# Kernel optimization log

Hardware: AMD Instinct MI355X
Metric: run time of the kernel (lower is better)

Reference implementation:

```python
import jax, jax.numpy as jnp
import numpy as np

D_MODEL = 512
D_STATE = 128
D_CONV = 4
EXPAND = 2
HEADDIM = 64
NGROUPS = 1
D_INNER = EXPAND * D_MODEL            # 1024
NHEADS = D_INNER // HEADDIM           # 16
CONV_DIM = D_INNER + 2 * NGROUPS * D_STATE   # 1280
D_IN_PROJ = 2 * D_INNER + 2 * NGROUPS * D_STATE + NHEADS  # 2320
EPS = 1e-5


def _silu(v):
    return v * jax.nn.sigmoid(v)


def setup_inputs() -> dict:
    key = jax.random.key(0)
    ks = jax.random.split(key, 8)
    B, L = 2, 1024
    x = jax.random.normal(ks[0], (B, L, D_MODEL), jnp.float32)
    in_proj_w = jax.random.normal(ks[1], (D_IN_PROJ, D_MODEL), jnp.float32) * (D_MODEL ** -0.5)
    conv_w = jax.random.normal(ks[2], (CONV_DIM, D_CONV), jnp.float32) * (D_CONV ** -0.5)
    conv_b = jnp.zeros((CONV_DIM,), jnp.float32)
    # dt_bias = softplus^-1(dt) for dt ~ U[1e-3, 0.1]  (Mamba2 init)
    dt = jax.random.uniform(ks[3], (NHEADS,), jnp.float32, 0.001, 0.1)
    dt_bias = jnp.log(jnp.expm1(dt))
    A_log = jnp.log(jax.random.uniform(ks[4], (NHEADS,), jnp.float32, 1.0, 16.0))
    D = jnp.ones((NHEADS,), jnp.float32)
    norm_w = jnp.ones((D_INNER,), jnp.float32)
    out_proj_w = jax.random.normal(ks[5], (D_MODEL, D_INNER), jnp.float32) * (D_INNER ** -0.5)
    return dict(x=x, in_proj_w=in_proj_w, conv_w=conv_w, conv_b=conv_b,
                dt_bias=dt_bias, A_log=A_log, D=D, norm_w=norm_w, out_proj_w=out_proj_w)


def _mamba2(x, in_proj_w, conv_w, conv_b, dt_bias, A_log, D, norm_w, out_proj_w):
    Bb, L, _ = x.shape
    # input projection -> [z | xBC | dt]
    zxbcdt = jnp.einsum('bld,ed->ble', x, in_proj_w)          # (B,L,2320)
    z = zxbcdt[..., :D_INNER]                                  # (B,L,1024)
    xBC = zxbcdt[..., D_INNER:D_INNER + CONV_DIM]              # (B,L,1280)
    dt = jax.nn.softplus(zxbcdt[..., D_INNER + CONV_DIM:] + dt_bias)  # (B,L,H)
    # causal depthwise conv1d over L + SiLU
    lhs = jnp.transpose(xBC, (0, 2, 1))                        # (B,C,L)
    rhs = conv_w[:, None, :]                                   # (C,1,K)
    conv = jax.lax.conv_general_dilated(
        lhs, rhs, window_strides=(1,), padding=[(D_CONV - 1, 0)],
        dimension_numbers=('NCH', 'OIH', 'NCH'), feature_group_count=CONV_DIM)
    xBC = _silu(jnp.transpose(conv, (0, 2, 1)) + conv_b)       # (B,L,1280)
    xs = xBC[..., :D_INNER].reshape(Bb, L, NHEADS, HEADDIM)    # (B,L,H,P)
    Bmat = xBC[..., D_INNER:D_INNER + D_STATE]                 # (B,L,N) ngroups=1
    Cmat = xBC[..., D_INNER + D_STATE:]                        # (B,L,N)
    # selective scan: h_t = exp(dt_t*A)*h_{t-1} + (dt_t*x_t) outer B_t ; y_t = C_t . h_t
    A = -jnp.exp(A_log)                                        # (H,)
    dA = jnp.exp(dt * A)                                       # (B,L,H)
    dx = dt[..., None] * xs                                    # (B,L,H,P)

    def step(h, inp):
        dA_t, dx_t, B_t, C_t = inp                             # (B,H),(B,H,P),(B,N),(B,N)
        h = h * dA_t[..., None, None] + dx_t[..., None] * B_t[:, None, None, :]
        y = jnp.einsum('bhpn,bn->bhp', h, C_t)
        return h, y

    h0 = jnp.zeros((Bb, NHEADS, HEADDIM, D_STATE), x.dtype)
    _, ys = jax.lax.scan(step, h0, (jnp.moveaxis(dA, 1, 0), jnp.moveaxis(dx, 1, 0),
                                    jnp.moveaxis(Bmat, 1, 0), jnp.moveaxis(Cmat, 1, 0)))
    y = jnp.moveaxis(ys, 0, 1) + xs * D[None, None, :, None]   # (B,L,H,P)
    y = y.reshape(Bb, L, D_INNER)
    # gated RMSNorm: rmsnorm(y * silu(z)) * w
    g = y * _silu(z)
    g = g * jax.lax.rsqrt(jnp.mean(g * g, axis=-1, keepdims=True) + EPS) * norm_w
    return jnp.einsum('ble,de->bld', g, out_proj_w)            # (B,L,d_model)


def reference(x, in_proj_w, conv_w, conv_b, dt_bias, A_log, D, norm_w, out_proj_w):
    return _mamba2(x, in_proj_w, conv_w, conv_b, dt_bias, A_log, D, norm_w, out_proj_w)
```

## Files before the change

kernel.cpp:

```cpp
#include <hip/hip_runtime.h>
#include <math.h>

#define BATCH 2
#define SEQ 1024
#define DM 512
#define DI 1024
#define DS 128
#define NH 16
#define HD 64
#define CONVD 1280
#define DPROJ 2320
#define ROWS (BATCH*SEQ)
#define NCH 16
#define CHK 64
#define NPAD 2432

typedef unsigned short u16;
typedef unsigned int   u32;
typedef u16   u16x4 __attribute__((ext_vector_type(4)));
typedef u16   u16x8 __attribute__((ext_vector_type(8)));
typedef short bf16x8 __attribute__((ext_vector_type(8)));
typedef float f32x4 __attribute__((ext_vector_type(4)));

__device__ __forceinline__ u16 f2bf(float f) {
    u32 u = __float_as_uint(f);
    return (u16)((u + 0x7fffu + ((u >> 16) & 1u)) >> 16);
}
__device__ __forceinline__ float bf2f(u16 h) {
    return __uint_as_float(((u32)h) << 16);
}
__device__ __forceinline__ void gl_lds16(const u16* g, u16* lds) {
    __builtin_amdgcn_global_load_lds((const __attribute__((address_space(1))) void*)g,
                                     (__attribute__((address_space(3))) void*)lds,
                                     16, 0, 0);
}

__device__ __forceinline__ int swz_off(int row, int q, int SLROW) {
    return (row*SLROW + (q ^ (row & 7)))*8;
}
template<int SLROW>
__device__ __forceinline__ void stage64(const u16* gbase, int gstride, u16* lds, int tid) {
    #pragma unroll
    for (int j = 0; j < (64*SLROW)/256; ++j) {
        int slot = j*256 + tid;
        int row = slot / SLROW;
        int pos = slot % SLROW;
        gl_lds16(gbase + (size_t)row*gstride + (pos ^ (row & 7))*8, lds + slot*8);
    }
}

__device__ __forceinline__ void cvt_blk(const float* __restrict__ src,
                                        u16* __restrict__ dst,
                                        int blk, int n_src, int n_total) {
    int idx = (blk*256 + threadIdx.x)*8;
    if (idx >= n_total) return;
    u16x8 o;
    if (idx + 8 <= n_src) {
        float4 a = *reinterpret_cast<const float4*>(src + idx);
        float4 b = *reinterpret_cast<const float4*>(src + idx + 4);
        o[0]=f2bf(a.x); o[1]=f2bf(a.y); o[2]=f2bf(a.z); o[3]=f2bf(a.w);
        o[4]=f2bf(b.x); o[5]=f2bf(b.y); o[6]=f2bf(b.z); o[7]=f2bf(b.w);
    } else {
        #pragma unroll
        for (int e = 0; e < 8; ++e)
            o[e] = (idx + e < n_src) ? f2bf(src[idx + e]) : (u16)0;
    }
    *reinterpret_cast<u16x8*>(dst + idx) = o;
}

__global__ __launch_bounds__(256) void k_prep(const float* __restrict__ x,
                                              const float* __restrict__ W,
                                              const float* __restrict__ Wo,
                                              const float* __restrict__ dt_bias,
                                              const float* __restrict__ A_log,
                                              u16* __restrict__ xb,
                                              u16* __restrict__ Wb,
                                              u16* __restrict__ Wob,
                                              float* __restrict__ dtb,
                                              float* __restrict__ abuf) {
    int bid = blockIdx.x;
    if (bid < 512) { cvt_blk(x, xb, bid, ROWS*DM, ROWS*DM); return; }
    if (bid < 1120) { cvt_blk(W, Wb, bid-512, DPROJ*DM, NPAD*DM); return; }
    if (bid < 1376) { cvt_blk(Wo, Wob, bid-1120, DM*DI, DM*DI); return; }
    int wave = threadIdx.x >> 6, lane = threadIdx.x & 63;
    int row = (bid-1376)*4 + wave;
    int h = lane & 15, part = lane >> 4;
    const float* xr = x + (size_t)row * DM + part*128;
    const float* wr = W + (size_t)(DI + CONVD + h) * DM + part*128;
    float acc = 0.f;
    #pragma unroll 4
    for (int j = 0; j < 32; ++j) {
        float4 xv = *reinterpret_cast<const float4*>(xr + j*4);
        float4 wv = *reinterpret_cast<const float4*>(wr + j*4);
        acc += xv.x*wv.x + xv.y*wv.y + xv.z*wv.z + xv.w*wv.w;
    }
    acc += __shfl_xor(acc, 16);
    acc += __shfl_xor(acc, 32);
    if (part == 0) {
        float v = acc + dt_bias[h];
        float dt = (v > 20.f) ? v : log1pf(expf(v));
        dtb[row*NH + h]  = dt;
        abuf[row*NH + h] = dt * (-expf(A_log[h]));
    }
}

template<int BM, int BN, int K, bool BF16OUT>
__global__ __launch_bounds__(256) void k_gemm(const u16* __restrict__ A,
                                              const u16* __restrict__ B,
                                              void* __restrict__ Cv,
                                              int ldc, int ncols) {
    constexpr int WTM = BM/2, WTN = BN/2, FM = WTM/16, FN = WTN/16;
    constexpr int CA = BM*4/256, CB = BN*4/256;
    __shared__ u16 As[BM*32];
    __shared__ u16 Bs[BN*32];
    int tid  = threadIdx.x;
    int lane = tid & 63, wave = tid >> 6;
    int wr = wave >> 1, wc = wave & 1;
    size_t bm = (size_t)blockIdx.y * BM, bn = (size_t)blockIdx.x * BN;

    const u16* srcA[CA]; u16* dstA[CA];
    #pragma unroll
    for (int j = 0; j < CA; ++j) {
        int i = j*256 + tid;
        int row = i >> 2, q = (i & 3) ^ ((row >> 1) & 3);
        srcA[j] = A + (bm + row) * (size_t)K + q*8;
        dstA[j] = As + i*8;
    }
    const u16* srcB[CB]; u16* dstB[CB];
    #pragma unroll
    for (int j = 0; j < CB; ++j) {
        int i = j*256 + tid;
        int row = i >> 2, q = (i & 3) ^ ((row >> 1) & 3);
        srcB[j] = B + (bn + row) * (size_t)K + q*8;
        dstB[j] = Bs + i*8;
    }

    int kq = lane >> 4;
    int aoff[FM], boff[FN];
    #pragma unroll
    for (int fi = 0; fi < FM; ++fi) {
        int row = wr*WTM + fi*16 + (lane & 15);
        aoff[fi] = (row*4 + (kq ^ ((row >> 1) & 3))) * 8;
    }
    #pragma unroll
    for (int fj = 0; fj < FN; ++fj) {
        int row = wc*WTN + fj*16 + (lane & 15);
        boff[fj] = (row*4 + (kq ^ ((row >> 1) & 3))) * 8;
    }

    f32x4 acc[FM][FN];
    #pragma unroll
    for (int fi = 0; fi < FM; ++fi)
        #pragma unroll
        for (int fj = 0; fj < FN; ++fj)
            acc[fi][fj] = (f32x4){0.f, 0.f, 0.f, 0.f};

    for (int k0 = 0; k0 < K; k0 += 32) {
        __syncthreads();
        #pragma unroll
        for (int j = 0; j < CA; ++j) gl_lds16(srcA[j] + k0, dstA[j]);
        #pragma unroll
        for (int j = 0; j < CB; ++j) gl_lds16(srcB[j] + k0, dstB[j]);
        __syncthreads();
        bf16x8 av[FM], bv[FN];
        #pragma unroll
        for (int fi = 0; fi < FM; ++fi)
            av[fi] = *reinterpret_cast<const bf16x8*>(As + aoff[fi]);
        #pragma unroll
        for (int fj = 0; fj < FN; ++fj)
            bv[fj] = *reinterpret_cast<const bf16x8*>(Bs + boff[fj]);
        #pragma unroll
        for (int fi = 0; fi < FM; ++fi)
            #pragma unroll
            for (int fj = 0; fj < FN; ++fj)
                acc[fi][fj] = __builtin_amdgcn_mfma_f32_16x16x32_bf16(
                    av[fi], bv[fj], acc[fi][fj], 0, 0, 0);
    }

    #pragma unroll
    for (int fi = 0; fi < FM; ++fi) {
        size_t grow0 = bm + wr*WTM + fi*16 + (lane >> 4)*4;
        #pragma unroll
        for (int fj = 0; fj < FN; ++fj) {
            size_t gcol = bn + wc*WTN + fj*16 + (lane & 15);
            if ((int)gcol < ncols) {
                #pragma unroll
                for (int r = 0; r < 4; ++r) {
                    if constexpr (BF16OUT)
                        ((u16*)Cv)[(grow0 + r)*ldc + gcol] = f2bf(acc[fi][fj][r]);
                    else
                        ((float*)Cv)[(grow0 + r)*ldc + gcol] = acc[fi][fj][r];
                }
            }
        }
    }
}

__global__ __launch_bounds__(320) void k_conv(const u16* __restrict__ zx,
                                              const float* __restrict__ cw,
                                              const float* __restrict__ cb,
                                              u16* __restrict__ convo) {
    int row = blockIdx.x;
    int l   = row & (SEQ-1);
    int c0  = threadIdx.x * 4;

    const float4* cw4 = reinterpret_cast<const float4*>(cw);
    float4 w0 = cw4[c0+0], w1 = cw4[c0+1], w2 = cw4[c0+2], w3 = cw4[c0+3];
    const float* wa0 = &w0.x; const float* wa1 = &w1.x;
    const float* wa2 = &w2.x; const float* wa3 = &w3.x;

    float4 bv = *reinterpret_cast<const float4*>(cb + c0);
    float acc0 = bv.x, acc1 = bv.y, acc2 = bv.z, acc3 = bv.w;

    #pragma unroll
    for (int k = 0; k < 4; ++k) {
        int lk = l - 3 + k;
        if (lk < 0) continue;
        u16x4 v = *reinterpret_cast<const u16x4*>(zx + (size_t)(row-3+k)*DPROJ + DI + c0);
        acc0 += bf2f(v[0]) * wa0[k];
        acc1 += bf2f(v[1]) * wa1[k];
        acc2 += bf2f(v[2]) * wa2[k];
        acc3 += bf2f(v[3]) * wa3[k];
    }
    u16x4 o;
    o[0] = f2bf(acc0 / (1.f + expf(-acc0)));
    o[1] = f2bf(acc1 / (1.f + expf(-acc1)));
    o[2] = f2bf(acc2 / (1.f + expf(-acc2)));
    o[3] = f2bf(acc3 / (1.f + expf(-acc3)));
    *reinterpret_cast<u16x4*>(convo + (size_t)row*CONVD + c0) = o;
}

__global__ __launch_bounds__(256) void k_chunk_state(
    const u16* __restrict__ convo, const float* __restrict__ dtb,
    const float* __restrict__ abuf, u16* __restrict__ Sb,
    float* __restrict__ Pbuf) {
    int blk = blockIdx.x;
    int c  = blk & (NCH-1);
    int h  = (blk >> 4) & (NH-1);
    int b  = blk >> 8;
    int row0 = b*SEQ + c*CHK;
    int tid = threadIdx.x, lane = tid & 63, wave = tid >> 6;
    int wr = wave >> 1, wc = wave & 1;

    __shared__ u16 xsT[64*64];
    __shared__ u16 BT[128*64];
    __shared__ float s_coef[CHK];

    int st = tid >> 2, q = tid & 3;
    const u16* r = convo + (size_t)(row0 + st)*CONVD;
    u16x8 xa = *reinterpret_cast<const u16x8*>(r + h*HD + q*16);
    u16x8 xc = *reinterpret_cast<const u16x8*>(r + h*HD + q*16 + 8);
    u16x8 b0 = *reinterpret_cast<const u16x8*>(r + DI + q*32);
    u16x8 b1 = *reinterpret_cast<const u16x8*>(r + DI + q*32 + 8);
    u16x8 b2 = *reinterpret_cast<const u16x8*>(r + DI + q*32 + 16);
    u16x8 b3 = *reinterpret_cast<const u16x8*>(r + DI + q*32 + 24);

    if (tid < CHK) {
        float v = abuf[(size_t)(row0 + tid)*NH + h];
        #pragma unroll
        for (int off = 1; off < 64; off <<= 1) {
            float o = __shfl_up(v, off);
            if (tid >= off) v += o;
        }
        float vend = __shfl(v, 63);
        float dt = dtb[(size_t)(row0 + tid)*NH + h];
        s_coef[tid] = dt * expf(vend - v);
        if (tid == 63) Pbuf[blk] = expf(vend);
    }
    __syncthreads();

    float cf = s_coef[st];
    #pragma unroll
    for (int e = 0; e < 16; ++e) {
        int p = q*16 + e;
        u16 xv = (e < 8) ? xa[e] : xc[e-8];
        xsT[(p*8 + ((st>>3) ^ (p&7)))*8 + (st&7)] = f2bf(cf * bf2f(xv));
    }
    #pragma unroll
    for (int e = 0; e < 32; ++e) {
        int n = q*32 + e;
        u16 bvv = (e < 8) ? b0[e] : (e < 16) ? b1[e-8] : (e < 24) ? b2[e-16] : b3[e-24];
        BT[(n*8 + ((st>>3) ^ (n&7)))*8 + (st&7)] = bvv;
    }
    __syncthreads();

    int kq = lane >> 4, fr = lane & 15;
    f32x4 acc[2][4];
    #pragma unroll
    for (int fi = 0; fi < 2; ++fi)
        #pragma unroll
        for (int fj = 0; fj < 4; ++fj)
            acc[fi][fj] = (f32x4){0.f,0.f,0.f,0.f};

    #pragma unroll
    for (int ks = 0; ks < 2; ++ks) {
        bf16x8 av[2], bv[4];
        #pragma unroll
        for (int fi = 0; fi < 2; ++fi)
            av[fi] = *reinterpret_cast<const bf16x8*>(xsT + swz_off(wr*32 + fi*16 + fr, ks*4 + kq, 8));
        #pragma unroll
        for (int fj = 0; fj < 4; ++fj)
            bv[fj] = *reinterpret_cast<const bf16x8*>(BT + swz_off(wc*64 + fj*16 + fr, ks*4 + kq, 8));
        #pragma unroll
        for (int fi = 0; fi < 2; ++fi)
            #pragma unroll
            for (int fj = 0; fj < 4; ++fj)
                acc[fi][fj] = __builtin_amdgcn_mfma_f32_16x16x32_bf16(av[fi], bv[fj], acc[fi][fj], 0,0,0);
    }

    u16* outp = Sb + (size_t)blk*(HD*DS);
    #pragma unroll
    for (int fi = 0; fi < 2; ++fi)
        #pragma unroll
        for (int rr = 0; rr < 4; ++rr) {
            int p = wr*32 + fi*16 + kq*4 + rr;
            #pragma unroll
            for (int fj = 0; fj < 4; ++fj) {
                int n = wc*64 + fj*16 + fr;
                outp[(size_t)p*DS + n] = f2bf(acc[fi][fj][rr]);
            }
        }
}

__global__ __launch_bounds__(256) void k_state_pass(u16* __restrict__ Sb,
                                                    const float* __restrict__ Pbuf) {
    int bh = blockIdx.x >> 3, seg = blockIdx.x & 7;
    int off = seg*1024 + threadIdx.x*4;
    u16x4 s[NCH];
    #pragma unroll
    for (int cc = 0; cc < NCH; ++cc)
        s[cc] = *reinterpret_cast<const u16x4*>(Sb + ((size_t)(bh*NCH + cc))*(HD*DS) + off);
    float hr[4] = {0.f,0.f,0.f,0.f};
    #pragma unroll
    for (int cc = 0; cc < NCH; ++cc) {
        u16x4 w = { f2bf(hr[0]), f2bf(hr[1]), f2bf(hr[2]), f2bf(hr[3]) };
        *reinterpret_cast<u16x4*>(Sb + ((size_t)(bh*NCH + cc))*(HD*DS) + off) = w;
        float P = Pbuf[bh*NCH + cc];
        #pragma unroll
        for (int j = 0; j < 4; ++j) hr[j] = hr[j]*P + bf2f(s[cc][j]);
    }
}

__global__ __launch_bounds__(256) void k_chunk_out(
    const u16* __restrict__ convo, const float* __restrict__ dtb,
    const float* __restrict__ abuf, const u16* __restrict__ Sb,
    const float* __restrict__ Dp, u16* __restrict__ ybuf) {
    int blk = blockIdx.x;
    int c  = blk & (NCH-1);
    int h  = (blk >> 4) & (NH-1);
    int b  = blk >> 8;
    int row0 = b*SEQ + c*CHK;
    int tid = threadIdx.x, lane = tid & 63, wave = tid >> 6;
    int wr = wave >> 1, wc = wave & 1;

    __shared__ u16 Ct[64*128];
    __shared__ u16 Bh[64*128];
    __shared__ u16 Mt[64*64];
    __shared__ u16 dxT[64*64];
    __shared__ float s_cum[CHK];
    __shared__ float s_dt[CHK];

    const u16* cbase = convo + (size_t)row0*CONVD;

    stage64<16>(cbase + DI + DS, CONVD, Ct, tid);
    stage64<16>(cbase + DI,      CONVD, Bh, tid);

    int st = tid >> 2, q = tid & 3;
    u16x8 xr0 = *reinterpret_cast<const u16x8*>(cbase + (size_t)st*CONVD + h*HD + q*16);
    u16x8 xr1 = *reinterpret_cast<const u16x8*>(cbase + (size_t)st*CONVD + h*HD + q*16 + 8);

    if (tid < CHK) {
        float v = abuf[(size_t)(row0 + tid)*NH + h];
        #pragma unroll
        for (int off = 1; off < 64; off <<= 1) {
            float o = __shfl_up(v, off);
            if (tid >= off) v += o;
        }
        s_cum[tid] = v;
        s_dt[tid] = dtb[(size_t)(row0 + tid)*NH + h];
    }
    __syncthreads();

    #pragma unroll
    for (int e = 0; e < 16; ++e) {
        int p = q*16 + e;
        u16 xv = (e < 8) ? xr0[e] : xr1[e-8];
        dxT[(p*8 + ((st>>3) ^ (p&7)))*8 + (st&7)] = xv;
    }

    int kq = lane >> 4, fr = lane & 15;

    f32x4 macc[2][2];
    #pragma unroll
    for (int fi = 0; fi < 2; ++fi)
        #pragma unroll
        for (int fj = 0; fj < 2; ++fj)
            macc[fi][fj] = (f32x4){0.f,0.f,0.f,0.f};
    #pragma unroll
    for (int ks = 0; ks < 4; ++ks) {
        bf16x8 av[2], bv[2];
        #pragma unroll
        for (int fi = 0; fi < 2; ++fi)
            av[fi] = *reinterpret_cast<const bf16x8*>(Ct + swz_off(wr*32 + fi*16 + fr, ks*4 + kq, 16));
        #pragma unroll
        for (int fj = 0; fj < 2; ++fj)
            bv[fj] = *reinterpret_cast<const bf16x8*>(Bh + swz_off(wc*32 + fj*16 + fr, ks*4 + kq, 16));
        #pragma unroll
        for (int fi = 0; fi < 2; ++fi)
            #pragma unroll
            for (int fj = 0; fj < 2; ++fj)
                macc[fi][fj] = __builtin_amdgcn_mfma_f32_16x16x32_bf16(av[fi], bv[fj], macc[fi][fj], 0,0,0);
    }

    #pragma unroll
    for (int fi = 0; fi < 2; ++fi)
        #pragma unroll
        for (int rr = 0; rr < 4; ++rr) {
            int t = wr*32 + fi*16 + kq*4 + rr;
            float cumt = s_cum[t];
            #pragma unroll
            for (int fj = 0; fj < 2; ++fj) {
                int s = wc*32 + fj*16 + fr;
                float val = (s <= t) ? macc[fi][fj][rr] * expf(cumt - s_cum[s]) * s_dt[s] : 0.f;
                Mt[(t*8 + ((s>>3) ^ (t&7)))*8 + (s&7)] = f2bf(val);
            }
        }
    __syncthreads();

    stage64<16>(Sb + (size_t)blk*(HD*DS), DS, Bh, tid);

    f32x4 accY[2][2];
    #pragma unroll
    for (int fi = 0; fi < 2; ++fi)
        #pragma unroll
        for (int fj = 0; fj < 2; ++fj)
            accY[fi][fj] = (f32x4){0.f,0.f,0.f,0.f};
    #pragma unroll
    for (int ks = 0; ks < 2; ++ks) {
        bf16x8 av[2], bv[2];
        #pragma unroll
        for (int fi = 0; fi < 2; ++fi)
            av[fi] = *reinterpret_cast<const bf16x8*>(Mt + swz_off(wr*32 + fi*16 + fr, ks*4 + kq, 8));
        #pragma unroll
        for (int fj = 0; fj < 2; ++fj)
            bv[fj] = *reinterpret_cast<const bf16x8*>(dxT + swz_off(wc*32 + fj*16 + fr, ks*4 + kq, 8));
        #pragma unroll
        for (int fi = 0; fi < 2; ++fi)
            #pragma unroll
            for (int fj = 0; fj < 2; ++fj)
                accY[fi][fj] = __builtin_amdgcn_mfma_f32_16x16x32_bf16(av[fi], bv[fj], accY[fi][fj], 0,0,0);
    }
    __syncthreads();

    f32x4 accD[2][2];
    #pragma unroll
    for (int fi = 0; fi < 2; ++fi)
        #pragma unroll
        for (int fj = 0; fj < 2; ++fj)
            accD[fi][fj] = (f32x4){0.f,0.f,0.f,0.f};
    #pragma unroll
    for (int ks = 0; ks < 4; ++ks) {
        bf16x8 av[2], bv[2];
        #pragma unroll
        for (int fi = 0; fi < 2; ++fi)
            av[fi] = *reinterpret_cast<const bf16x8*>(Ct + swz_off(wr*32 + fi*16 + fr, ks*4 + kq, 16));
        #pragma unroll
        for (int fj = 0; fj < 2; ++fj)
            bv[fj] = *reinterpret_cast<const bf16x8*>(Bh + swz_off(wc*32 + fj*16 + fr, ks*4 + kq, 16));
        #pragma unroll
        for (int fi = 0; fi < 2; ++fi)
            #pragma unroll
            for (int fj = 0; fj < 2; ++fj)
                accD[fi][fj] = __builtin_amdgcn_mfma_f32_16x16x32_bf16(av[fi], bv[fj], accD[fi][fj], 0,0,0);
    }

    float Dv = Dp[h];
    #pragma unroll
    for (int fi = 0; fi < 2; ++fi)
        #pragma unroll
        for (int rr = 0; rr < 4; ++rr) {
            int t = wr*32 + fi*16 + kq*4 + rr;
            float et = expf(s_cum[t]);
            #pragma unroll
            for (int fj = 0; fj < 2; ++fj) {
                int p = wc*32 + fj*16 + fr;
                float xs = bf2f(cbase[(size_t)t*CONVD + h*HD + p]);
                float y = accY[fi][fj][rr] + et*accD[fi][fj][rr] + Dv*xs;
                ybuf[(size_t)(row0 + t)*DI + h*HD + p] = f2bf(y);
            }
        }
}

__global__ __launch_bounds__(256) void k_gate(const u16* __restrict__ zx,
                                              const u16* __restrict__ ybuf,
                                              const float* __restrict__ nw,
                                              u16* __restrict__ g) {
    int row = blockIdx.x;
    int t = threadIdx.x;
    const u16* zr = zx + (size_t)row*DPROJ;
    const u16* yr = ybuf + (size_t)row*DI;

    u16x4 zv = *reinterpret_cast<const u16x4*>(zr + t*4);
    u16x4 yv = *reinterpret_cast<const u16x4*>(yr + t*4);
    float gv[4];
    float ss = 0.f;
    #pragma unroll
    for (int j = 0; j < 4; ++j) {
        float z = bf2f(zv[j]), y = bf2f(yv[j]);
        float sz = z / (1.f + expf(-z));
        float gg = y * sz;
        gv[j] = gg;
        ss += gg*gg;
    }
    ss += __shfl_xor(ss, 1);
    ss += __shfl_xor(ss, 2);
    ss += __shfl_xor(ss, 4);
    ss += __shfl_xor(ss, 8);
    ss += __shfl_xor(ss, 16);
    ss += __shfl_xor(ss, 32);
    __shared__ float ls[4];
    if ((t & 63) == 0) ls[t >> 6] = ss;
    __syncthreads();
    float tot = ls[0] + ls[1] + ls[2] + ls[3];
    float scale = rsqrtf(tot * (1.f/DI) + 1e-5f);

    float4 nv = *reinterpret_cast<const float4*>(nw + t*4);
    const float* na = &nv.x;
    u16x4 og = { f2bf(gv[0]*scale*na[0]), f2bf(gv[1]*scale*na[1]),
                 f2bf(gv[2]*scale*na[2]), f2bf(gv[3]*scale*na[3]) };
    *reinterpret_cast<u16x4*>(g + (size_t)row*DI + t*4) = og;
}

extern "C" void kernel_launch(void* const* d_in, const int* in_sizes, int n_in,
                              void* d_out, int out_size, void* d_ws, size_t ws_size,
                              hipStream_t stream) {
    const float* x         = (const float*)d_in[0];
    const float* in_proj_w = (const float*)d_in[1];
    const float* conv_w    = (const float*)d_in[2];
    const float* conv_b    = (const float*)d_in[3];
    const float* dt_bias   = (const float*)d_in[4];
    const float* A_log     = (const float*)d_in[5];
    const float* Dp        = (const float*)d_in[6];
    const float* norm_w    = (const float*)d_in[7];
    const float* out_proj_w= (const float*)d_in[8];
    float* out = (float*)d_out;

    char* p = (char*)d_ws;
    u16*   zxb   = (u16*)p;   p += (size_t)ROWS*DPROJ*2;
    u16*   convo = (u16*)p;   p += (size_t)ROWS*CONVD*2;
    float* dtb   = (float*)p; p += (size_t)ROWS*NH*4;
    float* abuf  = (float*)p; p += (size_t)ROWS*NH*4;
    u16*   ybuf  = (u16*)p;   p += (size_t)ROWS*DI*2;
    u16*   xb    = (u16*)p;   p += (size_t)ROWS*DM*2;
    u16*   Wb    = (u16*)p;   p += (size_t)NPAD*DM*2;
    u16*   Wob   = (u16*)p;   p += (size_t)DM*DI*2;
    u16*   Sb    = (u16*)p;   p += (size_t)BATCH*NH*NCH*HD*DS*2;
    float* Pbuf  = (float*)p; p += 512*4;
    u16*   gb    = (u16*)p;   p += (size_t)ROWS*DI*2;

    k_prep<<<1888, 256, 0, stream>>>(x, in_proj_w, out_proj_w, dt_bias, A_log,
                                     xb, Wb, Wob, dtb, abuf);

    k_gemm<64,128,512,true><<<dim3(NPAD/128, ROWS/64), 256, 0, stream>>>(xb, Wb, zxb, DPROJ, DPROJ);

    k_conv<<<ROWS, CONVD/4, 0, stream>>>(zxb, conv_w, conv_b, convo);

    k_chunk_state<<<BATCH*NH*NCH, 256, 0, stream>>>(convo, dtb, abuf, Sb, Pbuf);
    k_state_pass <<<BATCH*NH*8, 256, 0, stream>>>(Sb, Pbuf);
    k_chunk_out  <<<BATCH*NH*NCH, 256, 0, stream>>>(convo, dtb, abuf, Sb, Dp, ybuf);

    k_gate<<<ROWS, 256, 0, stream>>>(zxb, ybuf, norm_w, gb);

    k_gemm<64,64,1024,false><<<dim3(DM/64, ROWS/64), 256, 0, stream>>>(gb, Wob, out, DM, DM);
}
```

Before: 78.77 us.

## Double-buffer GEMM LDS tiles with BK=64 and prefetch next tile

Rewrites the bf16 MFMA GEMM main loop to use a K-tile of 64 instead of 32, with two LDS buffers so the global-to-LDS loads for the next tile are issued before computing the current one. It uses a single barrier per step instead of two and a wider XOR swizzle. The aim is to hide global load latency behind MFMA work and halve loop and sync overhead. In exchange, LDS use per block roughly quadruples, which may reduce occupancy.

```diff
diff --git a/kernel.cpp b/kernel.cpp
--- a/kernel.cpp
+++ b/kernel.cpp
@@ -109,80 +109,93 @@
                                               const u16* __restrict__ B,
                                               void* __restrict__ Cv,
                                               int ldc, int ncols) {
+    constexpr int BK = 64;
+    constexpr int NK = K / BK;
     constexpr int WTM = BM/2, WTN = BN/2, FM = WTM/16, FN = WTN/16;
-    constexpr int CA = BM*4/256, CB = BN*4/256;
-    __shared__ u16 As[BM*32];
-    __shared__ u16 Bs[BN*32];
-    int tid  = threadIdx.x;
-    int lane = tid & 63, wave = tid >> 6;
+    constexpr int CA = BM/32, CB = BN/32;
+    constexpr int TA = BM*8, TB = BN*8;
+    __shared__ u16 As[2*TA*8];
+    __shared__ u16 Bs[2*TB*8];
+    int tid = threadIdx.x, lane = tid & 63, wave = tid >> 6;
     int wr = wave >> 1, wc = wave & 1;
     size_t bm = (size_t)blockIdx.y * BM, bn = (size_t)blockIdx.x * BN;
 
-    const u16* srcA[CA]; u16* dstA[CA];
+    const u16* sA[CA]; int dA[CA];
     #pragma unroll
     for (int j = 0; j < CA; ++j) {
-        int i = j*256 + tid;
-        int row = i >> 2, q = (i & 3) ^ ((row >> 1) & 3);
-        srcA[j] = A + (bm + row) * (size_t)K + q*8;
-        dstA[j] = As + i*8;
-    }
-    const u16* srcB[CB]; u16* dstB[CB];
+        int i = j*256 + tid, row = i >> 3, pos = i & 7;
+        sA[j] = A + (bm + row)*(size_t)K + (pos ^ (row & 7))*8;
+        dA[j] = i*8;
+    }
+    const u16* sB[CB]; int dB[CB];
     #pragma unroll
     for (int j = 0; j < CB; ++j) {
-        int i = j*256 + tid;
-        int row = i >> 2, q = (i & 3) ^ ((row >> 1) & 3);
-        srcB[j] = B + (bn + row) * (size_t)K + q*8;
-        dstB[j] = Bs + i*8;
-    }
-
-    int kq = lane >> 4;
-    int aoff[FM], boff[FN];
+        int i = j*256 + tid, row = i >> 3, pos = i & 7;
+        sB[j] = B + (bn + row)*(size_t)K + (pos ^ (row & 7))*8;
+        dB[j] = i*8;
+    }
+
+    int fr = lane & 15, kq = lane >> 4;
+    int ar[FM], br[FN];
+    #pragma unroll
+    for (int fi = 0; fi < FM; ++fi) ar[fi] = wr*WTM + fi*16 + fr;
+    #pragma unroll
+    for (int fj = 0; fj < FN; ++fj) br[fj] = wc*WTN + fj*16 + fr;
+
+    f32x4 acc[FM][FN];
+    #pragma unroll
+    for (int fi = 0; fi < FM; ++fi)
+        #pragma unroll
+        for (int fj = 0; fj < FN; ++fj)
+            acc[fi][fj] = (f32x4){0.f,0.f,0.f,0.f};
+
+    #pragma unroll
+    for (int j = 0; j < CA; ++j) gl_lds16(sA[j], As + dA[j]);
+    #pragma unroll
+    for (int j = 0; j < CB; ++j) gl_lds16(sB[j], Bs + dB[j]);
+    asm volatile("s_waitcnt vmcnt(0)" ::: "memory");
+    __builtin_amdgcn_s_barrier();
+
+    int cur = 0;
+    #pragma unroll 1
+    for (int step = 0; step < NK; ++step) {
+        if (step + 1 < NK) {
+            int k0 = (step+1)*BK;
+            int nb = cur ^ 1;
+            #pragma unroll
+            for (int j = 0; j < CA; ++j) gl_lds16(sA[j] + k0, As + nb*TA*8 + dA[j]);
+            #pragma unroll
+            for (int j = 0; j < CB; ++j) gl_lds16(sB[j] + k0, Bs + nb*TB*8 + dB[j]);
+        }
+        const u16* Ab = As + cur*TA*8;
+        const u16* Bb = Bs + cur*TB*8;
+        #pragma unroll
+        for (int ks = 0; ks < 2; ++ks) {
+            bf16x8 av[FM], bv[FN];
+            #pragma unroll
+            for (int fi = 0; fi < FM; ++fi)
+                av[fi] = *reinterpret_cast<const bf16x8*>(Ab + (ar[fi]*8 + ((ks*4+kq) ^ (ar[fi]&7)))*8);
+            #pragma unroll
+            for (int fj = 0; fj < FN; ++fj)
+                bv[fj] = *reinterpret_cast<const bf16x8*>(Bb + (br[fj]*8 + ((ks*4+kq) ^ (br[fj]&7)))*8);
+            #pragma unroll
+            for (int fi = 0; fi < FM; ++fi)
+                #pragma unroll
+                for (int fj = 0; fj < FN; ++fj)
+                    acc[fi][fj] = __builtin_amdgcn_mfma_f32_16x16x32_bf16(
+                        av[fi], bv[fj], acc[fi][fj], 0, 0, 0);
+        }
+        asm volatile("s_waitcnt vmcnt(0)" ::: "memory");
+        __builtin_amdgcn_s_barrier();
+        cur ^= 1;
+    }
+
     #pragma unroll
     for (int fi = 0; fi < FM; ++fi) {
-        int row = wr*WTM + fi*16 + (lane & 15);
-        aoff[fi] = (row*4 + (kq ^ ((row >> 1) & 3))) * 8;
-    }
-    #pragma unroll
-    for (int fj = 0; fj < FN; ++fj) {
-        int row = wc*WTN + fj*16 + (lane & 15);
-        boff[fj] = (row*4 + (kq ^ ((row >> 1) & 3))) * 8;
-    }
-
-    f32x4 acc[FM][FN];
-    #pragma unroll
-    for (int fi = 0; fi < FM; ++fi)
-        #pragma unroll
-        for (int fj = 0; fj < FN; ++fj)
-            acc[fi][fj] = (f32x4){0.f, 0.f, 0.f, 0.f};
-
-    for (int k0 = 0; k0 < K; k0 += 32) {
-        __syncthreads();
-        #pragma unroll
-        for (int j = 0; j < CA; ++j) gl_lds16(srcA[j] + k0, dstA[j]);
-        #pragma unroll
-        for (int j = 0; j < CB; ++j) gl_lds16(srcB[j] + k0, dstB[j]);
-        __syncthreads();
-        bf16x8 av[FM], bv[FN];
-        #pragma unroll
-        for (int fi = 0; fi < FM; ++fi)
-            av[fi] = *reinterpret_cast<const bf16x8*>(As + aoff[fi]);
-        #pragma unroll
-        for (int fj = 0; fj < FN; ++fj)
-            bv[fj] = *reinterpret_cast<const bf16x8*>(Bs + boff[fj]);
-        #pragma unroll
-        for (int fi = 0; fi < FM; ++fi)
-            #pragma unroll
-            for (int fj = 0; fj < FN; ++fj)
-                acc[fi][fj] = __builtin_amdgcn_mfma_f32_16x16x32_bf16(
-                    av[fi], bv[fj], acc[fi][fj], 0, 0, 0);
-    }
-
-    #pragma unroll
-    for (int fi = 0; fi < FM; ++fi) {
-        size_t grow0 = bm + wr*WTM + fi*16 + (lane >> 4)*4;
+        size_t grow0 = bm + wr*WTM + fi*16 + kq*4;
         #pragma unroll
         for (int fj = 0; fj < FN; ++fj) {
-            size_t gcol = bn + wc*WTN + fj*16 + (lane & 15);
+            size_t gcol = bn + wc*WTN + fj*16 + fr;
             if ((int)gcol < ncols) {
                 #pragma unroll
                 for (int r = 0; r < 4; ++r) {
```

Result: faster. 76.24 us (-3.2%).
